# Performance work log

Hardware: AMD Instinct MI355X
Metric: run time of the kernel (lower is better)

The kernel has to match this reference:

```python
import jax, jax.numpy as jnp
import numpy as np

B, T, C, H = 8, 4096, 1024, 128  # batch, seq, n_embd, head_size


def setup_inputs() -> dict:
    key = jax.random.key(0)
    ks = jax.random.split(key, 4)
    std = 1.0 / np.sqrt(C)
    return {
        "x": jax.random.normal(ks[0], (B, T, C), dtype=jnp.float32),
        "Wq": jax.random.normal(ks[1], (C, H), dtype=jnp.float32) * std,
        "bq": jnp.zeros((H,), dtype=jnp.float32),
        "Wk": jax.random.normal(ks[2], (C, H), dtype=jnp.float32) * std,
        "bk": jnp.zeros((H,), dtype=jnp.float32),
        "Wv": jax.random.normal(ks[3], (C, H), dtype=jnp.float32) * std,
        "bv": jnp.zeros((H,), dtype=jnp.float32),
    }


def reference(x, Wq, bq, Wk, bk, Wv, bv):
    # Q, K, V projections: [B, T, H]
    q = x @ Wq + bq
    k = x @ Wk + bk
    v = x @ Wv + bv
    scale = jnp.asarray(H, x.dtype) ** -0.5
    # scaled attention scores: [B, T, T]
    wei = jnp.einsum("bqh,bkh->bqk", q, k) * scale
    # causal mask: position q attends to k <= q
    causal = jnp.tril(jnp.ones((T, T), dtype=bool))
    wei = jnp.where(causal[None, :, :], wei, jnp.finfo(x.dtype).min)
    wei = jax.nn.softmax(wei, axis=-1)
    # dropout p=0.0 (eval) -> identity
    out = jnp.einsum("bqk,bkh->bqh", wei, v)  # [B, T, H]
    return out
```

## Files before the change

kernel.cpp:

```cpp
#include <hip/hip_runtime.h>
#include <hip/hip_bf16.h>

typedef __attribute__((ext_vector_type(8))) short short8;
typedef __attribute__((ext_vector_type(4))) short shortx4;
typedef __attribute__((ext_vector_type(4))) float floatx4;
typedef __attribute__((ext_vector_type(4))) unsigned int uintx4;

#define BB 8
#define TT 4096
#define CC 1024
#define HH 128
#define BT (BB * TT)
#define MBASE 16.0f

__device__ __forceinline__ unsigned short f2bf(float f) {
    unsigned int u = __float_as_uint(f);
    u += 0x7fffu + ((u >> 16) & 1u);
    return (unsigned short)(u >> 16);
}

__device__ __forceinline__ void async16(const unsigned short* g, unsigned short* l) {
    __builtin_amdgcn_global_load_lds(
        (const __attribute__((address_space(1))) unsigned int*)g,
        (__attribute__((address_space(3))) unsigned int*)l, 16, 0, 0);
}

__global__ void conv_w(const float* __restrict__ Wq, const float* __restrict__ Wk,
                       const float* __restrict__ Wv, unsigned short* __restrict__ Wt) {
    __shared__ float tile[32][33];
    const int w = blockIdx.z, nt = blockIdx.y, kt = blockIdx.x;
    const int tx = threadIdx.x, ty = threadIdx.y;
    const float* W = (w == 0) ? Wq : ((w == 1) ? Wk : Wv);
#pragma unroll
    for (int i = 0; i < 4; ++i)
        tile[ty + 8 * i][tx] = W[(kt * 32 + ty + 8 * i) * HH + nt * 32 + tx];
    __syncthreads();
#pragma unroll
    for (int i = 0; i < 4; ++i)
        Wt[w * (HH * CC) + (nt * 32 + ty + 8 * i) * CC + kt * 32 + tx] = f2bf(tile[tx][ty + 8 * i]);
}

__global__ __launch_bounds__(256, 3) void proj_gemm(
    const float* __restrict__ x, const unsigned short* __restrict__ Wt,
    const float* __restrict__ bq, const float* __restrict__ bk, const float* __restrict__ bv,
    unsigned short* __restrict__ Qb, unsigned short* __restrict__ Kb,
    unsigned short* __restrict__ Vt) {
    __shared__ unsigned short Bs[2][96 * 64];
    const int gid = blockIdx.x;
    const int c = gid & 7, j = gid >> 3;
    const int mb = c * 32 + (j >> 2);
    const int nb = j & 3;
    const int tid = threadIdx.x, lane = tid & 63, wv = tid >> 6;
    const int quad = lane >> 4, l15 = lane & 15;
    const int brow = lane >> 3;
    const int wc = (lane & 7) ^ (brow & 7);
    const unsigned short* Wp = Wt + (long)nb * 96 * CC;
    const float* xw = x + ((long)mb * 128 + wv * 32 + l15) * CC + quad * 8;
    const int rw = mb * 128 + wv * 32;

    floatx4 acc[2][6];
#pragma unroll
    for (int i = 0; i < 2; ++i)
#pragma unroll
        for (int jj = 0; jj < 6; ++jj) {
            floatx4 z = {0.f, 0.f, 0.f, 0.f};
            acc[i][jj] = z;
        }

    floatx4 pf[8];
    short8 af[2][2];

    auto loadA = [&](int kt) {
#pragma unroll
        for (int mi = 0; mi < 2; ++mi)
#pragma unroll
            for (int ks = 0; ks < 2; ++ks) {
                const float* p = xw + (long)mi * 16 * CC + kt * 64 + ks * 32;
                pf[mi * 4 + ks * 2]     = *(const floatx4*)p;
                pf[mi * 4 + ks * 2 + 1] = *(const floatx4*)(p + 4);
            }
    };
    auto cvtA = [&]() {
#pragma unroll
        for (int mi = 0; mi < 2; ++mi)
#pragma unroll
            for (int ks = 0; ks < 2; ++ks) {
                floatx4 a = pf[mi * 4 + ks * 2], b2 = pf[mi * 4 + ks * 2 + 1];
                short8 r;
                r[0] = (short)f2bf(a[0]);  r[1] = (short)f2bf(a[1]);
                r[2] = (short)f2bf(a[2]);  r[3] = (short)f2bf(a[3]);
                r[4] = (short)f2bf(b2[0]); r[5] = (short)f2bf(b2[1]);
                r[6] = (short)f2bf(b2[2]); r[7] = (short)f2bf(b2[3]);
                af[mi][ks] = r;
            }
    };
    auto stageB = [&](int kt, int buf) {
#pragma unroll
        for (int h = 0; h < 3; ++h) {
            int grp = wv + 4 * h;
            async16(Wp + (long)(grp * 8 + brow) * CC + kt * 64 + wc * 8, &Bs[buf][grp * 512]);
        }
    };

    stageB(0, 0);
    __builtin_amdgcn_sched_barrier(0);
    loadA(0);
    __builtin_amdgcn_sched_barrier(0);
    asm volatile("s_waitcnt vmcnt(8)" ::: "memory");
    __builtin_amdgcn_s_barrier();
    int cur = 0;

    for (int kt = 0; kt < 16; ++kt) {
        const bool pfn = (kt < 15);
        if (pfn) stageB(kt + 1, cur ^ 1);
        __builtin_amdgcn_sched_barrier(0);
        cvtA();
        if (pfn) loadA(kt + 1);
        __builtin_amdgcn_sched_barrier(0);

#pragma unroll
        for (int ks = 0; ks < 2; ++ks)
#pragma unroll
            for (int ni = 0; ni < 6; ++ni) {
                short8 bfr = *(const short8*)&Bs[cur][(ni * 16 + l15) * 64 +
                                                      (((ks * 4 + quad) ^ (l15 & 7)) * 8)];
                acc[0][ni] = __builtin_amdgcn_mfma_f32_16x16x32_bf16(af[0][ks], bfr, acc[0][ni], 0, 0, 0);
                acc[1][ni] = __builtin_amdgcn_mfma_f32_16x16x32_bf16(af[1][ks], bfr, acc[1][ni], 0, 0, 0);
            }

        if (pfn) {
            __builtin_amdgcn_sched_barrier(0);
            asm volatile("s_waitcnt vmcnt(8)" ::: "memory");
            __builtin_amdgcn_s_barrier();
            cur ^= 1;
        }
    }

    const float qscale = 0.08838834764831845f * 1.4426950408889634f;
    unsigned short* Tw = &Bs[0][wv * 640];
#pragma unroll
    for (int ni = 0; ni < 6; ++ni) {
        int f = 6 * nb + ni;
        int col = f * 16 + l15;
        int h = col & 127;
        if (f < 16) {
            float bval = (f < 8) ? bq[h] : bk[h];
            unsigned short* dst = (f < 8) ? Qb : Kb;
#pragma unroll
            for (int mi = 0; mi < 2; ++mi)
#pragma unroll
                for (int r = 0; r < 4; ++r) {
                    int row = rw + mi * 16 + quad * 4 + r;
                    float v = acc[mi][ni][r] + bval;
                    if (f < 8) v *= qscale;
                    dst[(long)row * HH + h] = f2bf(v);
                }
        } else {
            float bval = bv[h];
#pragma unroll
            for (int mi = 0; mi < 2; ++mi) {
                shortx4 pk;
#pragma unroll
                for (int r = 0; r < 4; ++r) pk[r] = (short)f2bf(acc[mi][ni][r] + bval);
                *(shortx4*)&Tw[l15 * 40 + mi * 16 + quad * 4] = pk;
            }
            int th = lane >> 2, seg = lane & 3;
            uintx4 q0 = *(const uintx4*)&Tw[th * 40 + seg * 8];
            int hg = (f - 16) * 16 + th;
            int bb = rw >> 12, t0 = (rw & 4095) + seg * 8;
            unsigned short* vp = Vt + (long)bb * (HH * TT) + (long)hg * TT + t0;
            *(uintx4*)vp = q0;
        }
    }
}

__global__ __launch_bounds__(256) void attn(
    const unsigned short* __restrict__ Qb, const unsigned short* __restrict__ Kb,
    const unsigned short* __restrict__ Vt, unsigned short* __restrict__ Op,
    float* __restrict__ Lh) {
    __shared__ unsigned short Ks[64 * 128];
    __shared__ unsigned short Vs[128 * 64];
    __shared__ unsigned short Ps[4 * 16 * 40];
    const int gid = blockIdx.x;
    const int qb = 63 - (gid >> 5);
    const int sub = gid & 31;
    const int b = sub & 7;
    const int s = sub >> 3;
    const int len = qb + 1;
    const int lo = (s * len) >> 2;
    const int hi = ((s + 1) * len) >> 2;
    const int tid = threadIdx.x, lane = tid & 63, wv = tid >> 6;
    const int quad = lane >> 4, l15 = lane & 15;

    short8 qf[4];
    {
        const unsigned short* qp = Qb + ((long)b * TT + qb * 64 + wv * 16 + l15) * HH + quad * 8;
#pragma unroll
        for (int ks = 0; ks < 4; ++ks) qf[ks] = *(const short8*)(qp + ks * 32);
    }
    floatx4 o[8];
#pragma unroll
    for (int i = 0; i < 8; ++i) {
        floatx4 z = {0.f, 0.f, 0.f, 0.f};
        o[i] = z;
    }
    float l_part[4] = {0.f, 0.f, 0.f, 0.f};

    const int kc = l15 ^ (4 * wv + quad);
    const unsigned short* Kg = Kb + (long)b * TT * HH + ((long)lo * 64 + 4 * wv + quad) * HH + kc * 8;
    const int vrow = lane >> 3;
    const int vc = (lane & 7) ^ (vrow & 7);
    const unsigned short* Vg = Vt + (long)b * HH * TT + (long)(8 * wv + vrow) * TT + lo * 64 + vc * 8;
    unsigned short* Pw = &Ps[wv * 640];

    for (int kb = lo; kb < hi; ++kb) {
#pragma unroll
        for (int h = 0; h < 4; ++h) {
            int grp = 4 * h + wv;
            async16(Kg + (long)h * (16 * HH), &Ks[grp * 512]);
            async16(Vg + (long)h * 32 * TT, &Vs[grp * 512]);
        }
        Kg += (long)64 * HH;
        Vg += 64;
        __syncthreads();

        floatx4 sArr[4];
#pragma unroll
        for (int nt = 0; nt < 4; ++nt) {
            floatx4 z = {0.f, 0.f, 0.f, 0.f};
            sArr[nt] = z;
        }
        __builtin_amdgcn_s_setprio(1);
#pragma unroll
        for (int ks = 0; ks < 4; ++ks)
#pragma unroll
            for (int nt = 0; nt < 4; ++nt) {
                short8 kf = *(const short8*)&Ks[(nt * 16 + l15) * 128 + (((ks * 4 + quad) ^ l15) * 8)];
                sArr[nt] = __builtin_amdgcn_mfma_f32_16x16x32_bf16(qf[ks], kf, sArr[nt], 0, 0, 0);
            }
        __builtin_amdgcn_s_setprio(0);

        if (kb == qb) {
            int rowl = wv * 16 + quad * 4;
#pragma unroll
            for (int nt = 0; nt < 4; ++nt) {
                int col = nt * 16 + l15;
#pragma unroll
                for (int r = 0; r < 4; ++r)
                    if (col > rowl + r) sArr[nt][r] = -1e30f;
            }
        }

#pragma unroll
        for (int nt = 0; nt < 4; ++nt)
#pragma unroll
            for (int r = 0; r < 4; ++r)
                sArr[nt][r] = exp2f(sArr[nt][r] - MBASE);
#pragma unroll
        for (int r = 0; r < 4; ++r)
            l_part[r] += (sArr[0][r] + sArr[1][r]) + (sArr[2][r] + sArr[3][r]);

#pragma unroll
        for (int k2 = 0; k2 < 2; ++k2) {
#pragma unroll
            for (int ntl = 0; ntl < 2; ++ntl)
#pragma unroll
                for (int r = 0; r < 4; ++r)
                    Pw[(quad * 4 + r) * 40 + ntl * 16 + l15] = f2bf(sArr[k2 * 2 + ntl][r]);
            short8 pfrag = *(const short8*)&Pw[l15 * 40 + quad * 8];
            __builtin_amdgcn_s_setprio(1);
#pragma unroll
            for (int hn = 0; hn < 8; ++hn) {
                short8 vf = *(const short8*)&Vs[(hn * 16 + l15) * 64 +
                                                (((k2 * 4 + quad) ^ (l15 & 7)) * 8)];
                o[hn] = __builtin_amdgcn_mfma_f32_16x16x32_bf16(pfrag, vf, o[hn], 0, 0, 0);
            }
            __builtin_amdgcn_s_setprio(0);
        }
        __syncthreads();
    }

    long rbase = (long)b * TT + qb * 64 + wv * 16 + quad * 4;
    unsigned short* Os = Op + (long)s * BT * HH;
    if (hi > lo) {
#pragma unroll
        for (int hn = 0; hn < 8; ++hn)
#pragma unroll
            for (int r = 0; r < 4; ++r)
                Os[(rbase + r) * HH + hn * 16 + l15] = f2bf(o[hn][r]);
    }
#pragma unroll
    for (int r = 0; r < 4; ++r) {
        float l = l_part[r];
#pragma unroll
        for (int off = 1; off < 16; off <<= 1) l += __shfl_xor(l, off);
        if (l15 == 0) Lh[(long)s * BT + rbase + r] = (hi > lo) ? l : 0.f;
    }
}

__global__ __launch_bounds__(256) void merge_kern(
    const unsigned short* __restrict__ Op, const float* __restrict__ Lh,
    float* __restrict__ out) {
    long e = ((long)blockIdx.x * 256 + threadIdx.x) * 8;
    long row = e >> 7;
    float lsum = Lh[row] + Lh[BT + row] + Lh[2 * (long)BT + row] + Lh[3 * (long)BT + row];
    float inv = 1.f / lsum;
    float acc[8];
#pragma unroll
    for (int j = 0; j < 8; ++j) acc[j] = 0.f;
#pragma unroll
    for (int s = 0; s < 4; ++s) {
        float ls = Lh[(long)s * BT + row];
        if (ls > 0.f) {
            uintx4 p = *(const uintx4*)(Op + (long)s * BT * HH + e);
#pragma unroll
            for (int j = 0; j < 4; ++j) {
                acc[2 * j]     += __uint_as_float(p[j] << 16);
                acc[2 * j + 1] += __uint_as_float(p[j] & 0xffff0000u);
            }
        }
    }
    floatx4 o0, o1;
#pragma unroll
    for (int j = 0; j < 4; ++j) {
        if (j < 2) { o0[2 * j] = acc[2 * j] * inv; o0[2 * j + 1] = acc[2 * j + 1] * inv; }
        else { o1[2 * (j - 2)] = acc[2 * j] * inv; o1[2 * (j - 2) + 1] = acc[2 * j + 1] * inv; }
    }
    *(floatx4*)(out + e) = o0;
    *(floatx4*)(out + e + 4) = o1;
}

extern "C" void kernel_launch(void* const* d_in, const int* in_sizes, int n_in,
                              void* d_out, int out_size, void* d_ws, size_t ws_size,
                              hipStream_t stream) {
    const float* x  = (const float*)d_in[0];
    const float* Wq = (const float*)d_in[1];
    const float* bq = (const float*)d_in[2];
    const float* Wk = (const float*)d_in[3];
    const float* bk = (const float*)d_in[4];
    const float* Wv = (const float*)d_in[5];
    const float* bv = (const float*)d_in[6];
    float* out = (float*)d_out;

    char* ws = (char*)d_ws;
    unsigned short* Wt = (unsigned short*)(ws);
    unsigned short* Qb = (unsigned short*)(ws + 1048576);
    unsigned short* Kb = (unsigned short*)(ws + 9437184);
    unsigned short* Vt = (unsigned short*)(ws + 17825792);
    unsigned short* Op = (unsigned short*)(ws + 26214400);
    float*          Lh = (float*)(ws + 59768832);

    conv_w<<<dim3(32, 4, 3), dim3(32, 8), 0, stream>>>(Wq, Wk, Wv, Wt);
    proj_gemm<<<1024, 256, 0, stream>>>(x, Wt, bq, bk, bv, Qb, Kb, Vt);
    attn<<<2048, 256, 0, stream>>>(Qb, Kb, Vt, Op, Lh);
    merge_kern<<<2048, 256, 0, stream>>>(Op, Lh, out);
}
```

Measured before the change: 322.4 us.

## Widen projection N-tile with triple buffering and pair query blocks in attention

The projection GEMM now computes 192 output columns per block instead of 96, so each x tile is loaded and converted once for twice as many columns. It halves the grid and moves to a three-stage async B pipeline with adjusted waitcnts. The attention kernel runs 512-thread blocks that handle two adjacent query blocks sharing each staged K/V tile, which halves K/V global traffic per query row; waves whose query block is past the diagonal skip compute. The costs are more registers and LDS in the GEMM (occupancy hint drops to 2), and more imbalance inside attention blocks near the causal boundary.

Measured after the change: 291.0 us. 1.11x faster.

```diff
diff --git a/kernel.cpp b/kernel.cpp
--- a/kernel.cpp
+++ b/kernel.cpp
@@ -40,29 +40,29 @@
         Wt[w * (HH * CC) + (nt * 32 + ty + 8 * i) * CC + kt * 32 + tx] = f2bf(tile[tx][ty + 8 * i]);
 }
 
-__global__ __launch_bounds__(256, 3) void proj_gemm(
+__global__ __launch_bounds__(256, 2) void proj_gemm(
     const float* __restrict__ x, const unsigned short* __restrict__ Wt,
     const float* __restrict__ bq, const float* __restrict__ bk, const float* __restrict__ bv,
     unsigned short* __restrict__ Qb, unsigned short* __restrict__ Kb,
     unsigned short* __restrict__ Vt) {
-    __shared__ unsigned short Bs[2][96 * 64];
+    __shared__ unsigned short Bs[3][192 * 64];
     const int gid = blockIdx.x;
     const int c = gid & 7, j = gid >> 3;
-    const int mb = c * 32 + (j >> 2);
-    const int nb = j & 3;
+    const int mb = c * 32 + (j >> 1);
+    const int nb = j & 1;
     const int tid = threadIdx.x, lane = tid & 63, wv = tid >> 6;
     const int quad = lane >> 4, l15 = lane & 15;
     const int brow = lane >> 3;
     const int wc = (lane & 7) ^ (brow & 7);
-    const unsigned short* Wp = Wt + (long)nb * 96 * CC;
+    const unsigned short* Wp = Wt + (long)nb * 192 * CC;
     const float* xw = x + ((long)mb * 128 + wv * 32 + l15) * CC + quad * 8;
     const int rw = mb * 128 + wv * 32;
 
-    floatx4 acc[2][6];
+    floatx4 acc[2][12];
 #pragma unroll
     for (int i = 0; i < 2; ++i)
 #pragma unroll
-        for (int jj = 0; jj < 6; ++jj) {
+        for (int jj = 0; jj < 12; ++jj) {
             floatx4 z = {0.f, 0.f, 0.f, 0.f};
             acc[i][jj] = z;
         }
@@ -96,51 +96,57 @@
     };
     auto stageB = [&](int kt, int buf) {
 #pragma unroll
-        for (int h = 0; h < 3; ++h) {
+        for (int h = 0; h < 6; ++h) {
             int grp = wv + 4 * h;
             async16(Wp + (long)(grp * 8 + brow) * CC + kt * 64 + wc * 8, &Bs[buf][grp * 512]);
         }
     };
 
+    loadA(0);
     stageB(0, 0);
+    stageB(1, 1);
     __builtin_amdgcn_sched_barrier(0);
-    loadA(0);
+    asm volatile("s_waitcnt vmcnt(6)" ::: "memory");
+    __builtin_amdgcn_s_barrier();
     __builtin_amdgcn_sched_barrier(0);
-    asm volatile("s_waitcnt vmcnt(8)" ::: "memory");
-    __builtin_amdgcn_s_barrier();
     int cur = 0;
 
     for (int kt = 0; kt < 16; ++kt) {
-        const bool pfn = (kt < 15);
-        if (pfn) stageB(kt + 1, cur ^ 1);
+        cvtA();
+        if (kt < 15) loadA(kt + 1);
         __builtin_amdgcn_sched_barrier(0);
-        cvtA();
-        if (pfn) loadA(kt + 1);
+        if (kt < 14) {
+            int b2 = cur ? cur - 1 : 2;
+            stageB(kt + 2, b2);
+        }
         __builtin_amdgcn_sched_barrier(0);
 
+        const unsigned short* Bc = Bs[cur];
 #pragma unroll
         for (int ks = 0; ks < 2; ++ks)
 #pragma unroll
-            for (int ni = 0; ni < 6; ++ni) {
-                short8 bfr = *(const short8*)&Bs[cur][(ni * 16 + l15) * 64 +
-                                                      (((ks * 4 + quad) ^ (l15 & 7)) * 8)];
+            for (int ni = 0; ni < 12; ++ni) {
+                short8 bfr = *(const short8*)&Bc[(ni * 16 + l15) * 64 +
+                                                 (((ks * 4 + quad) ^ (l15 & 7)) * 8)];
                 acc[0][ni] = __builtin_amdgcn_mfma_f32_16x16x32_bf16(af[0][ks], bfr, acc[0][ni], 0, 0, 0);
                 acc[1][ni] = __builtin_amdgcn_mfma_f32_16x16x32_bf16(af[1][ks], bfr, acc[1][ni], 0, 0, 0);
             }
-
-        if (pfn) {
+        __builtin_amdgcn_sched_barrier(0);
+
+        if (kt < 15) {
+            if (kt < 14) { asm volatile("s_waitcnt vmcnt(14)" ::: "memory"); }
+            else         { asm volatile("s_waitcnt vmcnt(8)"  ::: "memory"); }
+            __builtin_amdgcn_s_barrier();
             __builtin_amdgcn_sched_barrier(0);
-            asm volatile("s_waitcnt vmcnt(8)" ::: "memory");
-            __builtin_amdgcn_s_barrier();
-            cur ^= 1;
+            cur = (cur == 2) ? 0 : cur + 1;
         }
     }
 
     const float qscale = 0.08838834764831845f * 1.4426950408889634f;
-    unsigned short* Tw = &Bs[0][wv * 640];
-#pragma unroll
-    for (int ni = 0; ni < 6; ++ni) {
-        int f = 6 * nb + ni;
+    unsigned short* Tw = &Bs[1][wv * 640];
+#pragma unroll
+    for (int ni = 0; ni < 12; ++ni) {
+        int f = 12 * nb + ni;
         int col = f * 16 + l15;
         int h = col & 127;
         if (f < 16) {
@@ -174,29 +180,32 @@
     }
 }
 
-__global__ __launch_bounds__(256) void attn(
+__global__ __launch_bounds__(512, 2) void attn(
     const unsigned short* __restrict__ Qb, const unsigned short* __restrict__ Kb,
     const unsigned short* __restrict__ Vt, unsigned short* __restrict__ Op,
     float* __restrict__ Lh) {
     __shared__ unsigned short Ks[64 * 128];
     __shared__ unsigned short Vs[128 * 64];
-    __shared__ unsigned short Ps[4 * 16 * 40];
+    __shared__ unsigned short Ps[8 * 16 * 40];
     const int gid = blockIdx.x;
-    const int qb = 63 - (gid >> 5);
-    const int sub = gid & 31;
-    const int b = sub & 7;
-    const int s = sub >> 3;
-    const int len = qb + 1;
-    const int lo = (s * len) >> 2;
-    const int hi = ((s + 1) * len) >> 2;
+    const int b = gid & 7;
+    const int idx = gid >> 3;
+    const int qp = idx >> 2;
+    const int s = idx & 3;
+    const int qb0 = 62 - 2 * qp;
+    const int len2 = qb0 + 2;
+    const int lo = (s * len2) >> 2;
+    const int hi = ((s + 1) * len2) >> 2;
     const int tid = threadIdx.x, lane = tid & 63, wv = tid >> 6;
     const int quad = lane >> 4, l15 = lane & 15;
+    const int qb_w = qb0 + (wv >> 2);
+    const int hi_eff = (hi < qb_w + 1) ? hi : qb_w + 1;
 
     short8 qf[4];
     {
-        const unsigned short* qp = Qb + ((long)b * TT + qb * 64 + wv * 16 + l15) * HH + quad * 8;
-#pragma unroll
-        for (int ks = 0; ks < 4; ++ks) qf[ks] = *(const short8*)(qp + ks * 32);
+        const unsigned short* qp_ = Qb + ((long)b * TT + qb0 * 64 + wv * 16 + l15) * HH + quad * 8;
+#pragma unroll
+        for (int ks = 0; ks < 4; ++ks) qf[ks] = *(const short8*)(qp_ + ks * 32);
     }
     floatx4 o[8];
 #pragma unroll
@@ -206,83 +215,85 @@
     }
     float l_part[4] = {0.f, 0.f, 0.f, 0.f};
 
-    const int kc = l15 ^ (4 * wv + quad);
+    const int kc = l15 ^ ((4 * wv + quad) & 15);
     const unsigned short* Kg = Kb + (long)b * TT * HH + ((long)lo * 64 + 4 * wv + quad) * HH + kc * 8;
     const int vrow = lane >> 3;
-    const int vc = (lane & 7) ^ (vrow & 7);
+    const int vc = (lane & 7) ^ vrow;
     const unsigned short* Vg = Vt + (long)b * HH * TT + (long)(8 * wv + vrow) * TT + lo * 64 + vc * 8;
     unsigned short* Pw = &Ps[wv * 640];
 
     for (int kb = lo; kb < hi; ++kb) {
 #pragma unroll
-        for (int h = 0; h < 4; ++h) {
-            int grp = 4 * h + wv;
-            async16(Kg + (long)h * (16 * HH), &Ks[grp * 512]);
-            async16(Vg + (long)h * 32 * TT, &Vs[grp * 512]);
+        for (int h = 0; h < 2; ++h) {
+            int grp = 8 * h + wv;
+            async16(Kg + (long)h * 32 * HH, &Ks[grp * 512]);
+            async16(Vg + (long)h * 64 * TT, &Vs[grp * 512]);
         }
         Kg += (long)64 * HH;
         Vg += 64;
         __syncthreads();
 
-        floatx4 sArr[4];
-#pragma unroll
-        for (int nt = 0; nt < 4; ++nt) {
-            floatx4 z = {0.f, 0.f, 0.f, 0.f};
-            sArr[nt] = z;
-        }
-        __builtin_amdgcn_s_setprio(1);
-#pragma unroll
-        for (int ks = 0; ks < 4; ++ks)
+        if (kb <= qb_w) {
+            floatx4 sArr[4];
 #pragma unroll
             for (int nt = 0; nt < 4; ++nt) {
-                short8 kf = *(const short8*)&Ks[(nt * 16 + l15) * 128 + (((ks * 4 + quad) ^ l15) * 8)];
-                sArr[nt] = __builtin_amdgcn_mfma_f32_16x16x32_bf16(qf[ks], kf, sArr[nt], 0, 0, 0);
-            }
-        __builtin_amdgcn_s_setprio(0);
-
-        if (kb == qb) {
-            int rowl = wv * 16 + quad * 4;
-#pragma unroll
-            for (int nt = 0; nt < 4; ++nt) {
-                int col = nt * 16 + l15;
+                floatx4 z = {0.f, 0.f, 0.f, 0.f};
+                sArr[nt] = z;
+            }
+            __builtin_amdgcn_s_setprio(1);
+#pragma unroll
+            for (int ks = 0; ks < 4; ++ks)
+#pragma unroll
+                for (int nt = 0; nt < 4; ++nt) {
+                    short8 kf = *(const short8*)&Ks[(nt * 16 + l15) * 128 + (((ks * 4 + quad) ^ l15) * 8)];
+                    sArr[nt] = __builtin_amdgcn_mfma_f32_16x16x32_bf16(qf[ks], kf, sArr[nt], 0, 0, 0);
+                }
+            __builtin_amdgcn_s_setprio(0);
+
+            if (kb == qb_w) {
+                int rowl = (wv & 3) * 16 + quad * 4;
+#pragma unroll
+                for (int nt = 0; nt < 4; ++nt) {
+                    int col = nt * 16 + l15;
+#pragma unroll
+                    for (int r = 0; r < 4; ++r)
+                        if (col > rowl + r) sArr[nt][r] = -1e30f;
+                }
+            }
+
+#pragma unroll
+            for (int nt = 0; nt < 4; ++nt)
 #pragma unroll
                 for (int r = 0; r < 4; ++r)
-                    if (col > rowl + r) sArr[nt][r] = -1e30f;
-            }
-        }
-
-#pragma unroll
-        for (int nt = 0; nt < 4; ++nt)
+                    sArr[nt][r] = exp2f(sArr[nt][r] - MBASE);
 #pragma unroll
             for (int r = 0; r < 4; ++r)
-                sArr[nt][r] = exp2f(sArr[nt][r] - MBASE);
-#pragma unroll
-        for (int r = 0; r < 4; ++r)
-            l_part[r] += (sArr[0][r] + sArr[1][r]) + (sArr[2][r] + sArr[3][r]);
-
-#pragma unroll
-        for (int k2 = 0; k2 < 2; ++k2) {
-#pragma unroll
-            for (int ntl = 0; ntl < 2; ++ntl)
-#pragma unroll
-                for (int r = 0; r < 4; ++r)
-                    Pw[(quad * 4 + r) * 40 + ntl * 16 + l15] = f2bf(sArr[k2 * 2 + ntl][r]);
-            short8 pfrag = *(const short8*)&Pw[l15 * 40 + quad * 8];
-            __builtin_amdgcn_s_setprio(1);
-#pragma unroll
-            for (int hn = 0; hn < 8; ++hn) {
-                short8 vf = *(const short8*)&Vs[(hn * 16 + l15) * 64 +
-                                                (((k2 * 4 + quad) ^ (l15 & 7)) * 8)];
-                o[hn] = __builtin_amdgcn_mfma_f32_16x16x32_bf16(pfrag, vf, o[hn], 0, 0, 0);
-            }
-            __builtin_amdgcn_s_setprio(0);
+                l_part[r] += (sArr[0][r] + sArr[1][r]) + (sArr[2][r] + sArr[3][r]);
+
+#pragma unroll
+            for (int k2 = 0; k2 < 2; ++k2) {
+#pragma unroll
+                for (int ntl = 0; ntl < 2; ++ntl)
+#pragma unroll
+                    for (int r = 0; r < 4; ++r)
+                        Pw[(quad * 4 + r) * 40 + ntl * 16 + l15] = f2bf(sArr[k2 * 2 + ntl][r]);
+                short8 pfrag = *(const short8*)&Pw[l15 * 40 + quad * 8];
+                __builtin_amdgcn_s_setprio(1);
+#pragma unroll
+                for (int hn = 0; hn < 8; ++hn) {
+                    short8 vf = *(const short8*)&Vs[(hn * 16 + l15) * 64 +
+                                                    (((k2 * 4 + quad) ^ (l15 & 7)) * 8)];
+                    o[hn] = __builtin_amdgcn_mfma_f32_16x16x32_bf16(pfrag, vf, o[hn], 0, 0, 0);
+                }
+                __builtin_amdgcn_s_setprio(0);
+            }
         }
         __syncthreads();
     }
 
-    long rbase = (long)b * TT + qb * 64 + wv * 16 + quad * 4;
+    long rbase = (long)b * TT + qb0 * 64 + wv * 16 + quad * 4;
     unsigned short* Os = Op + (long)s * BT * HH;
-    if (hi > lo) {
+    if (hi_eff > lo) {
 #pragma unroll
         for (int hn = 0; hn < 8; ++hn)
 #pragma unroll
@@ -294,7 +305,7 @@
         float l = l_part[r];
 #pragma unroll
         for (int off = 1; off < 16; off <<= 1) l += __shfl_xor(l, off);
-        if (l15 == 0) Lh[(long)s * BT + rbase + r] = (hi > lo) ? l : 0.f;
+        if (l15 == 0) Lh[(long)s * BT + rbase + r] = (hi_eff > lo) ? l : 0.f;
     }
 }
 
@@ -351,7 +362,7 @@
     float*          Lh = (float*)(ws + 59768832);
 
     conv_w<<<dim3(32, 4, 3), dim3(32, 8), 0, stream>>>(Wq, Wk, Wv, Wt);
-    proj_gemm<<<1024, 256, 0, stream>>>(x, Wt, bq, bk, bv, Qb, Kb, Vt);
-    attn<<<2048, 256, 0, stream>>>(Qb, Kb, Vt, Op, Lh);
+    proj_gemm<<<512, 256, 0, stream>>>(x, Wt, bq, bk, bv, Qb, Kb, Vt);
+    attn<<<1024, 512, 0, stream>>>(Qb, Kb, Vt, Op, Lh);
     merge_kern<<<2048, 256, 0, stream>>>(Op, Lh, out);
 }
```
